# Optimization experiments

Measured on AMD Instinct MI355X. Metric: run time of the kernel, lower is better.

The kernel has to match this reference:

```python
import jax, jax.numpy as jnp
import numpy as np

B, M, N, K = 2, 25000, 100000, 16
HID, DIM, NGROUPS = 64, 64, 8
GN_EPS = 1e-5


def conv1x1(x, w, b):
    # x: [B,C,M,K], w: [O,C], b: [O]
    return jnp.einsum('bcmk,oc->bomk', x, w) + b[None, :, None, None]


def group_norm(x, gamma, beta, ngroups):
    b, c, m, k = x.shape
    xg = x.reshape(b, ngroups, c // ngroups, m, k)
    mu = xg.mean(axis=(2, 3, 4), keepdims=True)
    var = xg.var(axis=(2, 3, 4), keepdims=True)
    xn = ((xg - mu) / jnp.sqrt(var + GN_EPS)).reshape(b, c, m, k)
    return xn * gamma[None, :, None, None] + beta[None, :, None, None]


def mlp(x, w1, b1, g, be, w2, b2):
    h = jax.nn.relu(group_norm(conv1x1(x, w1, b1), g, be, NGROUPS))
    return conv1x1(h, w2, b2)


def setup_inputs() -> dict:
    key = jax.random.key(0)
    ks = jax.random.split(key, 16)
    inp = {
        'q_xyzs': jax.random.normal(ks[0], (B, 3, M), jnp.float32),
        'k_xyzs': jax.random.normal(ks[1], (B, 3, N), jnp.float32),
        'knn_idx': jax.random.randint(ks[2], (B, M, K), 0, N),
        'mask': jax.random.randint(ks[3], (B, M, K), 0, 2).astype(bool),
        # embed_positions MLP params
        'pe_w1': jax.random.normal(ks[4], (HID, 4), jnp.float32) * 0.05,
        'pe_b1': jnp.zeros((HID,), jnp.float32),
        'pe_g': jnp.ones((HID,), jnp.float32),
        'pe_be': jnp.zeros((HID,), jnp.float32),
        'pe_w2': jax.random.normal(ks[5], (DIM, HID), jnp.float32) * 0.05,
        'pe_b2': jnp.zeros((DIM,), jnp.float32),
        # attention MLP params
        'at_w1': jax.random.normal(ks[6], (HID, DIM), jnp.float32) * 0.05,
        'at_b1': jnp.zeros((HID,), jnp.float32),
        'at_g': jnp.ones((HID,), jnp.float32),
        'at_be': jnp.zeros((HID,), jnp.float32),
        'at_w2': jax.random.normal(ks[7], (DIM, HID), jnp.float32) * 0.05,
        'at_b2': jnp.zeros((DIM,), jnp.float32),
    }
    return inp


def reference(q_xyzs, k_xyzs, knn_idx, mask,
              pe_w1, pe_b1, pe_g, pe_be, pe_w2, pe_b2,
              at_w1, at_b1, at_g, at_be, at_w2, at_b2):
    # gather KNN coordinates: [B,3,M,K]
    knn_xyzs = jax.vmap(lambda pts, idx: pts[:, idx])(k_xyzs, knn_idx)
    offset = knn_xyzs - q_xyzs[..., None]
    dist = jnp.linalg.norm(offset, axis=1, keepdims=True)  # [B,1,M,K]
    direction = offset / jnp.maximum(dist, 1e-12)
    local_pattern = jnp.concatenate([direction, dist], axis=1)  # [B,4,M,K]

    pe = mlp(local_pattern, pe_w1, pe_b1, pe_g, pe_be, pe_w2, pe_b2)  # [B,DIM,M,K]
    attn = mlp(pe, at_w1, at_b1, at_g, at_be, at_w2, at_b2)
    mask_value = -jnp.finfo(attn.dtype).max
    attn = jnp.where(mask[:, None], attn, mask_value)
    attn = jax.nn.softmax(attn, axis=-1)
    return (pe * attn).sum(axis=-1)  # [B,DIM,M]
```

## Files before the change

### kernel.cpp

```cpp
#include <hip/hip_runtime.h>

#define Bn 2
#define Mn 25000
#define Nn 100000
#define MK 400000
#define GN_EPS 1e-5f
#define NEG_BIG (-3.402823466e+38f)
#define LOG2E 1.44269504088896340736f

#define G1 512
#define G2 512

#define BEFF_OFF 0
#define B1P_OFF  64
#define AB1P_OFF 192
#define AB2L_OFF 320
#define WF16_OFF 384
#define AW1P_OFF 6528
#define W1F_OFF  10624
#define MSK_OFF  11136
#define SP_OFF   36160
#define YP_OFF   52544
#define YS_OFF   183616
#define KXT_OFF  184128
#define QT_OFF   984128
#define XF_OFF   1184128

typedef _Float16 hf8 __attribute__((ext_vector_type(8)));
typedef _Float16 hf4 __attribute__((ext_vector_type(4)));
typedef _Float16 hf2 __attribute__((ext_vector_type(2)));
typedef float f32x16 __attribute__((ext_vector_type(16)));

__device__ __forceinline__ f32x16 mfma16(hf8 a, hf8 b, f32x16 c) {
    return __builtin_amdgcn_mfma_f32_32x32x16_f16(a, b, c, 0, 0, 0);
}
__device__ __forceinline__ f32x16 splat16(float v) {
    f32x16 x;
#pragma unroll
    for (int r = 0; r < 16; ++r) x[r] = v;
    return x;
}
__device__ __forceinline__ hf8 zero8() {
    hf8 z;
#pragma unroll
    for (int j = 0; j < 8; ++j) z[j] = (_Float16)0.f;
    return z;
}
__device__ __forceinline__ hf2 pkcvt(float a, float b) {
    return __builtin_bit_cast(hf2, __builtin_amdgcn_cvt_pkrtz(a, b));
}
__device__ __forceinline__ hf2 pkrelu(hf2 v) {
    hf2 z; z[0] = (_Float16)0.f; z[1] = (_Float16)0.f;
    return __builtin_elementwise_max(v, z);
}
__device__ __forceinline__ float waveSum(float v) {
#pragma unroll
    for (int s = 32; s; s >>= 1) v += __shfl_down(v, s, 64);
    return v;
}
#define ROWFN(r, lane) (((r) & 3) + 8*((r) >> 2) + 4*((lane) >> 5))

__global__ __launch_bounds__(256) void prep0_kernel(
    const float* __restrict__ q, const float* __restrict__ kx,
    float* __restrict__ ws)
{
    float4* kxt = (float4*)(ws + KXT_OFF);
    float4* qt  = (float4*)(ws + QT_OFF);
    for (int e = blockIdx.x*256 + threadIdx.x; e < 2*Nn; e += gridDim.x*256) {
        const int b = e / Nn, n = e % Nn;
        float4 v;
        v.x = kx[(b*3+0)*Nn + n]; v.y = kx[(b*3+1)*Nn + n];
        v.z = kx[(b*3+2)*Nn + n]; v.w = 0.f;
        kxt[e] = v;
    }
    for (int e = blockIdx.x*256 + threadIdx.x; e < 2*Mn; e += gridDim.x*256) {
        const int b = e / Mn, m = e % Mn;
        float4 v;
        v.x = q[(b*3+0)*Mn + m]; v.y = q[(b*3+1)*Mn + m];
        v.z = q[(b*3+2)*Mn + m]; v.w = 0.f;
        qt[e] = v;
    }
}

__global__ __launch_bounds__(256) void gatherx_kernel(
    const int* __restrict__ idx, const int* __restrict__ mask,
    float* __restrict__ ws)
{
    __shared__ float red[4][16];
    const int b = blockIdx.y;
    const float4* kxt = (const float4*)(ws + KXT_OFF) + (size_t)b*Nn;
    const float4* qt  = (const float4*)(ws + QT_OFF)  + (size_t)b*Mn;
    _Float16* xf = (_Float16*)(ws + XF_OFF);
    unsigned short* m16 = (unsigned short*)(ws + MSK_OFF) + (size_t)b*25024;
    float v[14];
#pragma unroll
    for (int j = 0; j < 14; ++j) v[j] = 0.f;

    for (int i = blockIdx.x*256 + threadIdx.x; i < MK; i += G1*256) {
        const int mm = i >> 4;
        const int id = idx[(size_t)b*MK + i];
        const float4 kv = kxt[id];
        const float4 qv = qt[mm];
        const float ox = kv.x - qv.x, oy = kv.y - qv.y, oz = kv.z - qv.z;
        const float d  = sqrtf(ox*ox + oy*oy + oz*oz);
        const float inv = 1.0f / fmaxf(d, 1e-12f);
        const float x0 = ox*inv, x1 = oy*inv, x2 = oz*inv, x3 = d;

        const hf2 lo = pkcvt(x0, x1);
        const hf2 hi = pkcvt(x2, x3);
        hf4 pk;
        pk[0] = lo[0]; pk[1] = lo[1]; pk[2] = hi[0]; pk[3] = hi[1];
        *(hf4*)&xf[((size_t)b*MK + i)*4] = pk;

        const unsigned long long mb = __ballot(mask[(size_t)b*MK + i] != 0);
        if ((threadIdx.x & 63) == 0)
            *(unsigned long long*)&m16[i >> 4] = mb;

        v[0] += x0; v[1] += x1; v[2] += x2; v[3] += x3;
        v[4] += x0*x0; v[5] += x0*x1; v[6] += x0*x2; v[7] += x0*x3;
        v[8] += x1*x1; v[9] += x1*x2; v[10] += x1*x3;
        v[11] += x2*x2; v[12] += x2*x3; v[13] += x3*x3;
    }
    const int lane = threadIdx.x & 63, wv = threadIdx.x >> 6;
#pragma unroll
    for (int j = 0; j < 14; ++j) v[j] = waveSum(v[j]);
    if (lane == 0) {
#pragma unroll
        for (int j = 0; j < 14; ++j) red[wv][j] = v[j];
    }
    __syncthreads();
    if (threadIdx.x < 14)
        ws[SP_OFF + ((size_t)b*G1 + blockIdx.x)*16 + threadIdx.x] =
            red[0][threadIdx.x] + red[1][threadIdx.x] + red[2][threadIdx.x] + red[3][threadIdx.x];
}

__global__ void prep1_kernel(
    const float* __restrict__ ws_r,
    const float* __restrict__ w1, const float* __restrict__ b1,
    const float* __restrict__ g1, const float* __restrict__ be1,
    const float* __restrict__ w2, const float* __restrict__ pe_b2,
    const float* __restrict__ aw1, const float* __restrict__ ab1,
    const float* __restrict__ aw2, const float* __restrict__ ab2,
    float* __restrict__ ws)
{
    const int t = threadIdx.x;
    _Float16* WF = (_Float16*)(ws + WF16_OFF);

    if (blockIdx.x > 0) {
        const int e = (blockIdx.x - 1)*256 + t;
        const int o = e >> 6, c = e & 63;
        WF[e]        = (_Float16)w2[e];
        WF[4096 + e] = (_Float16)(aw2[e] * LOG2E);
        float acc = 0.f;
        for (int d = 0; d < 64; ++d) acc = fmaf(aw1[o*64 + d], w2[d*64 + c], acc);
        WF[8192 + e] = (_Float16)acc;
        return;
    }

    __shared__ double S[2][14];
    __shared__ float Eh[2][64], Eq[2][64];

    if (t < 28) {
        const int b = t / 14, j = t % 14;
        const float* p = ws_r + SP_OFF + (size_t)b*G1*16 + j;
        double acc = 0.0;
        for (int g = 0; g < G1; g += 4)
            acc += (double)p[(g+0)*16] + (double)p[(g+1)*16]
                 + (double)p[(g+2)*16] + (double)p[(g+3)*16];
        S[b][j] = acc;
    }
    __syncthreads();

    if (t < 128) {
        const int b = t >> 6, o = t & 63;
        const double inv = 1.0 / (double)MK;
        double mu[4];
#pragma unroll
        for (int c = 0; c < 4; ++c) mu[c] = S[b][c] * inv;
        double m2[4][4];
        {
            const int map[4][4] = {{0,1,2,3},{1,4,5,6},{2,5,7,8},{3,6,8,9}};
#pragma unroll
            for (int c = 0; c < 4; ++c)
#pragma unroll
                for (int c2 = 0; c2 < 4; ++c2)
                    m2[c][c2] = S[b][4 + map[c][c2]] * inv;
        }
        double w[4];
#pragma unroll
        for (int c = 0; c < 4; ++c) w[c] = (double)w1[o*4 + c];
        double s = 0.0, qd = 0.0;
#pragma unroll
        for (int c = 0; c < 4; ++c) {
            s += w[c] * mu[c];
#pragma unroll
            for (int c2 = 0; c2 < 4; ++c2) qd += w[c]*w[c2]*m2[c][c2];
        }
        const double bb = (double)b1[o];
        Eh[b][o] = (float)(s + bb);
        Eq[b][o] = (float)(qd + 2.0*bb*s + bb*bb);
    }
    __syncthreads();
    if (t < 128) {
        const int b = t >> 6, o = t & 63, g = o & ~7;
        float mg = 0.f, qg = 0.f;
#pragma unroll
        for (int j = 0; j < 8; ++j) { mg += Eh[b][g + j]; qg += Eq[b][g + j]; }
        mg *= 0.125f; qg *= 0.125f;
        const float var = fmaxf(qg - mg*mg, 0.f);
        const float a = g1[o] / sqrtf(var + GN_EPS);
        const float c1v = be1[o] - mg*a;
        _Float16* W1F = (_Float16*)(ws + W1F_OFF);
        hf8 wrow;
#pragma unroll
        for (int c = 0; c < 4; ++c) wrow[c] = (_Float16)(a * w1[o*4 + c]);
#pragma unroll
        for (int c = 4; c < 8; ++c) wrow[c] = (_Float16)0.f;
        *(hf8*)&W1F[(b*64 + o)*8] = wrow;
        ws[B1P_OFF + b*64 + o] = fmaf(a, b1[o], c1v);
    }
    if (t < 64) {
        float acc = ab1[t];
        for (int d = 0; d < 64; ++d) acc = fmaf(aw1[t*64 + d], pe_b2[d], acc);
        ws[BEFF_OFF + t] = acc;
    } else if (t < 128) {
        ws[AB2L_OFF + (t - 64)] = ab2[t - 64] * LOG2E;
    }
}

__global__ __launch_bounds__(256, 4) void pass2_kernel(
    const float* __restrict__ cws, float* __restrict__ ws)
{
    __shared__ __align__(16) _Float16 Xs[4][32][72];
    const int b = blockIdx.y;
    const int tid = threadIdx.x, lane = tid & 63, wv = tid >> 6;
    const int colA = lane & 31;
    const int klo = (lane >> 5) * 8;
    const _Float16* xf  = (const _Float16*)(cws + XF_OFF);
    const _Float16* WFe = (const _Float16*)(cws + WF16_OFF) + 8192;
    const _Float16* W1F = (const _Float16*)(cws + W1F_OFF);

    hf8 BW[2][4];
#pragma unroll
    for (int jc = 0; jc < 2; ++jc)
#pragma unroll
        for (int ks = 0; ks < 4; ++ks)
            BW[jc][ks] = *(const hf8*)&WFe[(2*colA + jc)*64 + 16*ks + klo];
    hf8 BX[2];
    if (klo == 0) {
        BX[0] = *(const hf8*)&W1F[(b*64 + 2*colA)*8];
        BX[1] = *(const hf8*)&W1F[(b*64 + 2*colA + 1)*8];
    } else { BX[0] = zero8(); BX[1] = zero8(); }
    const float bias0 = cws[B1P_OFF + b*64 + 2*colA];
    const float bias1 = cws[B1P_OFF + b*64 + 2*colA + 1];

    float sh[2] = {0.f, 0.f}, sq[2] = {0.f, 0.f};

    for (int base = blockIdx.x * 128; base < MK; base += G2 * 128) {
        const int pt0 = base + 32*wv;
        hf8 ax = zero8();
        if (klo == 0) {
            hf4 xv = *(const hf4*)&xf[((size_t)b*MK + pt0 + colA)*4];
#pragma unroll
            for (int j = 0; j < 4; ++j) ax[j] = xv[j];
        }
        f32x16 r0 = splat16(bias0), r1t = splat16(bias1);
        r0  = mfma16(ax, BX[0], r0);
        r1t = mfma16(ax, BX[1], r1t);
#pragma unroll
        for (int r = 0; r < 16; ++r) {
            const int row = ROWFN(r, lane);
            *(hf2*)&Xs[wv][row][2*colA] = pkrelu(pkcvt(r0[r], r1t[r]));
        }
        hf8 A[4];
#pragma unroll
        for (int ks = 0; ks < 4; ++ks)
            A[ks] = *(const hf8*)&Xs[wv][colA][16*ks + klo];
#pragma unroll
        for (int jc = 0; jc < 2; ++jc) {
            f32x16 C = splat16(0.f);
#pragma unroll
            for (int ks = 0; ks < 4; ++ks) C = mfma16(A[ks], BW[jc][ks], C);
#pragma unroll
            for (int r = 0; r < 16; ++r) {
                const float vy = C[r];
                sh[jc] += vy;
                sq[jc] = fmaf(vy, vy, sq[jc]);
            }
        }
    }

#pragma unroll
    for (int jc = 0; jc < 2; ++jc) {
        sh[jc] += __shfl_xor(sh[jc], 32, 64);
        sq[jc] += __shfl_xor(sq[jc], 32, 64);
    }
    __syncthreads();
    float* red = (float*)Xs;
    if (lane < 32) {
#pragma unroll
        for (int jc = 0; jc < 2; ++jc) {
            red[wv*128 +      2*colA + jc] = sh[jc];
            red[wv*128 + 64 + 2*colA + jc] = sq[jc];
        }
    }
    __syncthreads();
    if (tid < 128) {
        const float v = red[tid] + red[128 + tid] + red[256 + tid] + red[384 + tid];
        ws[YP_OFF + ((size_t)b*G2 + blockIdx.x)*128 + tid] = v;
    }
}

__global__ __launch_bounds__(64) void prep2a_kernel(
    const float* __restrict__ ws_r, float* __restrict__ ws)
{
    const int o2 = blockIdx.x;
    const int b = o2 >> 7, i = o2 & 127;
    const float* p = ws_r + YP_OFF + (size_t)b*G2*128 + i;
    double acc = 0.0;
    for (int g = threadIdx.x; g < G2; g += 64) acc += (double)p[(size_t)g*128];
#pragma unroll
    for (int s = 32; s; s >>= 1) acc += __shfl_down(acc, s, 64);
    if (threadIdx.x == 0) ((double*)(ws + YS_OFF))[o2] = acc;
}

__global__ void prep2b_kernel(const float* __restrict__ ws_r,
                              const float* __restrict__ g2, const float* __restrict__ be2,
                              const float* __restrict__ aw1, const float* __restrict__ ab1,
                              float* __restrict__ ws)
{
    __shared__ float EH[2][64], EQ[2][64];
    __shared__ float A2s[2][64];
    const int t = threadIdx.x;
    const double* YS = (const double*)(ws_r + YS_OFF);
    if (t < 128) {
        const int b = t >> 6, o = t & 63;
        const double invMK = 1.0 / (double)MK;
        const double my = YS[b*128 + o] * invMK;
        const double qy = YS[b*128 + 64 + o] * invMK;
        const double beff = (double)ws_r[BEFF_OFF + o];
        EH[b][o] = (float)(my + beff);
        EQ[b][o] = (float)(qy + 2.0*beff*my + beff*beff);
    }
    __syncthreads();
    if (t < 128) {
        const int b = t >> 6, o = t & 63, g = o & ~7;
        float mg = 0.f, qg = 0.f;
#pragma unroll
        for (int j = 0; j < 8; ++j) { mg += EH[b][g + j]; qg += EQ[b][g + j]; }
        mg *= 0.125f; qg *= 0.125f;
        const float var = fmaxf(qg - mg*mg, 0.f);
        const float a = g2[o] / sqrtf(var + GN_EPS);
        A2s[b][o] = a;
        ws[AB1P_OFF + b*64 + o] = fmaf(a, ab1[o], be2[o] - mg*a);
    }
    __syncthreads();
    _Float16* AW1P = (_Float16*)(ws + AW1P_OFF);
    for (int e = t; e < 8192; e += 256) {
        const int b = e >> 12, oc = e & 4095, o = oc >> 6;
        AW1P[e] = (_Float16)(A2s[b][o] * aw1[oc]);
    }
}

__global__ __launch_bounds__(256, 4) void pass3_kernel(
    const float* __restrict__ b2,
    const float* __restrict__ cws, float* __restrict__ out)
{
    __shared__ __align__(16) _Float16 Xs[4][32][72];
    float* O = (float*)Xs;

    const int b = blockIdx.y;
    const int base = blockIdx.x * 128;
    const int tid = threadIdx.x;
    const int lane = tid & 63, wv = tid >> 6;
    const int colA = lane & 31;
    const int klo = (lane >> 5) * 8;
    const int pt0 = base + 32*wv;

    const _Float16* xf   = (const _Float16*)(cws + XF_OFF);
    const _Float16* WF   = (const _Float16*)(cws + WF16_OFF);
    const _Float16* AW1P = (const _Float16*)(cws + AW1P_OFF) + (size_t)b*4096;
    const _Float16* W1F  = (const _Float16*)(cws + W1F_OFF);
    const unsigned mb32 = *(const unsigned*)((const unsigned short*)(cws + MSK_OFF)
                                             + (size_t)b*25024 + (pt0 >> 4));
    const unsigned mbs = __builtin_amdgcn_readfirstlane(mb32);

    {
        hf8 ax = zero8();
        hf8 BX0, BX1;
        if (klo == 0) {
            hf4 xv = *(const hf4*)&xf[((size_t)b*MK + pt0 + colA)*4];
#pragma unroll
            for (int j = 0; j < 4; ++j) ax[j] = xv[j];
            BX0 = *(const hf8*)&W1F[(b*64 + 2*colA)*8];
            BX1 = *(const hf8*)&W1F[(b*64 + 2*colA + 1)*8];
        } else { BX0 = zero8(); BX1 = zero8(); }
        f32x16 r0  = splat16(cws[B1P_OFF + b*64 + 2*colA]);
        f32x16 r1t = splat16(cws[B1P_OFF + b*64 + 2*colA + 1]);
        r0  = mfma16(ax, BX0, r0);
        r1t = mfma16(ax, BX1, r1t);
#pragma unroll
        for (int r = 0; r < 16; ++r) {
            const int row = ROWFN(r, lane);
            *(hf2*)&Xs[wv][row][2*colA] = pkrelu(pkcvt(r0[r], r1t[r]));
        }
    }
    if (lane < 32) {
        hf8 pad = zero8();
        pad[0] = ((mb32 >> lane) & 1u) ? (_Float16)0.f : (_Float16)(-60000.f);
        *(hf8*)&Xs[wv][lane][64] = pad;
    }

    f32x16 pe0 = splat16(b2[2*colA]);
    f32x16 pe1 = splat16(b2[2*colA + 1]);
#pragma unroll
    for (int ks = 0; ks < 4; ++ks) {
        const int off = 16*ks + klo;
        hf8 a   = *(const hf8*)&Xs[wv][colA][off];
        hf8 b0f = *(const hf8*)&WF[(2*colA)*64 + off];
        hf8 b1f = *(const hf8*)&WF[(2*colA + 1)*64 + off];
        pe0 = mfma16(a, b0f, pe0);
        pe1 = mfma16(a, b1f, pe1);
    }
#pragma unroll
    for (int r = 0; r < 16; ++r) {
        const int row = ROWFN(r, lane);
        *(hf2*)&Xs[wv][row][2*colA] = pkcvt(pe0[r], pe1[r]);
    }

    f32x16 h0 = splat16(cws[AB1P_OFF + b*64 + 2*colA]);
    f32x16 h1 = splat16(cws[AB1P_OFF + b*64 + 2*colA + 1]);
#pragma unroll
    for (int ks = 0; ks < 4; ++ks) {
        const int off = 16*ks + klo;
        hf8 a   = *(const hf8*)&Xs[wv][colA][off];
        hf8 b0f = *(const hf8*)&AW1P[(2*colA)*64 + off];
        hf8 b1f = *(const hf8*)&AW1P[(2*colA + 1)*64 + off];
        h0 = mfma16(a, b0f, h0);
        h1 = mfma16(a, b1f, h1);
    }
#pragma unroll
    for (int r = 0; r < 16; ++r) {
        const int row = ROWFN(r, lane);
        *(hf2*)&Xs[wv][row][2*colA] = pkrelu(pkcvt(h0[r], h1[r]));
    }

    f32x16 l0 = splat16(cws[AB2L_OFF + 2*colA]);
    f32x16 l1 = splat16(cws[AB2L_OFF + 2*colA + 1]);
#pragma unroll
    for (int ks = 0; ks < 4; ++ks) {
        const int off = 16*ks + klo;
        hf8 a   = *(const hf8*)&Xs[wv][colA][off];
        hf8 b0f = *(const hf8*)&WF[4096 + (2*colA)*64 + off];
        hf8 b1f = *(const hf8*)&WF[4096 + (2*colA + 1)*64 + off];
        l0 = mfma16(a, b0f, l0);
        l1 = mfma16(a, b1f, l1);
    }
    {
        hf8 a5 = zero8(), b5 = zero8();
        if (klo == 0) {
            a5 = *(const hf8*)&Xs[wv][colA][64];
            b5[0] = (_Float16)1.f;
        }
        l0 = mfma16(a5, b5, l0);
        l1 = mfma16(a5, b5, l1);
    }

    __syncthreads();

    {
        auto softmax_tile = [&](const f32x16& lg, const f32x16& pe, int j) {
#pragma unroll
            for (int mh = 0; mh < 2; ++mh) {
                float mx = lg[8*mh];
#pragma unroll
                for (int rr = 1; rr < 8; ++rr) mx = fmaxf(mx, lg[8*mh + rr]);
                mx = fmaxf(mx, __shfl_xor(mx, 32, 64));
                float se, sw = 0.f;
                if (((mbs >> (16*mh)) & 0xFFFFu) != 0u) {
                    se = 0.f;
#pragma unroll
                    for (int rr = 0; rr < 8; ++rr) {
                        const float e = exp2f(lg[8*mh + rr] - mx);
                        se += e;
                        sw = fmaf(e, pe[8*mh + rr], sw);
                    }
                } else {
                    se = 8.f;
#pragma unroll
                    for (int rr = 0; rr < 8; ++rr) sw += pe[8*mh + rr];
                }
                se += __shfl_xor(se, 32, 64);
                sw += __shfl_xor(sw, 32, 64);
                if (lane < 32)
                    O[(2*lane + j)*9 + (2*wv + mh)] = sw * __builtin_amdgcn_rcpf(se);
            }
        };
        softmax_tile(l0, pe0, 0);
        softmax_tile(l1, pe1, 1);
    }
    __syncthreads();

    if (tid < 128) {
        const int o = tid >> 1, mq = (tid & 1) * 4;
        float4 v;
        v.x = O[o*9 + mq];     v.y = O[o*9 + mq + 1];
        v.z = O[o*9 + mq + 2]; v.w = O[o*9 + mq + 3];
        *(float4*)&out[((size_t)b*64 + o)*Mn + blockIdx.x*8 + mq] = v;
    }
}

extern "C" void kernel_launch(void* const* d_in, const int* in_sizes, int n_in,
                              void* d_out, int out_size, void* d_ws, size_t ws_size,
                              hipStream_t stream) {
    (void)in_sizes; (void)n_in; (void)out_size; (void)ws_size;
    const float* q    = (const float*)d_in[0];
    const float* kx   = (const float*)d_in[1];
    const int*   idx  = (const int*)  d_in[2];
    const int*   mask = (const int*)  d_in[3];
    const float* w1   = (const float*)d_in[4];
    const float* b1   = (const float*)d_in[5];
    const float* g1   = (const float*)d_in[6];
    const float* be1  = (const float*)d_in[7];
    const float* w2   = (const float*)d_in[8];
    const float* b2   = (const float*)d_in[9];
    const float* aw1  = (const float*)d_in[10];
    const float* ab1  = (const float*)d_in[11];
    const float* g2   = (const float*)d_in[12];
    const float* be2  = (const float*)d_in[13];
    const float* aw2  = (const float*)d_in[14];
    const float* ab2  = (const float*)d_in[15];
    float* out = (float*)d_out;
    float* ws  = (float*)d_ws;

    prep0_kernel<<<256, 256, 0, stream>>>(q, kx, ws);
    gatherx_kernel<<<dim3(G1, Bn), 256, 0, stream>>>(idx, mask, ws);
    prep1_kernel<<<17, 256, 0, stream>>>(ws, w1, b1, g1, be1, w2, b2, aw1, ab1, aw2, ab2, ws);
    pass2_kernel<<<dim3(G2, Bn), 256, 0, stream>>>(ws, ws);
    prep2a_kernel<<<256, 64, 0, stream>>>(ws, ws);
    prep2b_kernel<<<1, 256, 0, stream>>>(ws, g2, be2, aw1, ab1, ws);
    pass3_kernel<<<dim3(MK/128, Bn), 256, 0, stream>>>(b2, ws, out);
}
```

Before: 221.7 us.

## Process two 32-point tiles per wave in pass3 to reuse weight fragments

Each wave in the final fused MLP/softmax kernel now handles two 32-row tiles (256 points per block instead of 128). The weight B-fragments loaded from global memory are reused across both tiles, and the pe values are kept in packed half registers instead of fp32 accumulators. This halves the grid size and the per-point weight loads, at the cost of more registers (launch bounds reduced to 3 blocks per CU), double the shared memory, and a bounds-checked tail block.

```diff
diff --git a/kernel.cpp b/kernel.cpp
--- a/kernel.cpp
+++ b/kernel.cpp
@@ -362,114 +362,153 @@
     }
 }
 
-__global__ __launch_bounds__(256, 4) void pass3_kernel(
+__global__ __launch_bounds__(256, 3) void pass3_kernel(
     const float* __restrict__ b2,
     const float* __restrict__ cws, float* __restrict__ out)
 {
-    __shared__ __align__(16) _Float16 Xs[4][32][72];
+    __shared__ __align__(16) _Float16 Xs[8][32][72];
     float* O = (float*)Xs;
 
     const int b = blockIdx.y;
-    const int base = blockIdx.x * 128;
+    const int base = blockIdx.x * 256;
     const int tid = threadIdx.x;
     const int lane = tid & 63, wv = tid >> 6;
     const int colA = lane & 31;
     const int klo = (lane >> 5) * 8;
-    const int pt0 = base + 32*wv;
 
     const _Float16* xf   = (const _Float16*)(cws + XF_OFF);
     const _Float16* WF   = (const _Float16*)(cws + WF16_OFF);
     const _Float16* AW1P = (const _Float16*)(cws + AW1P_OFF) + (size_t)b*4096;
     const _Float16* W1F  = (const _Float16*)(cws + W1F_OFF);
-    const unsigned mb32 = *(const unsigned*)((const unsigned short*)(cws + MSK_OFF)
-                                             + (size_t)b*25024 + (pt0 >> 4));
-    const unsigned mbs = __builtin_amdgcn_readfirstlane(mb32);
+    const unsigned short* m16 = (const unsigned short*)(cws + MSK_OFF) + (size_t)b*25024;
+
+    int pt0[2];
+    pt0[0] = base + 64*wv;
+    pt0[1] = base + 64*wv + 32;
+    unsigned mb[2];
+#pragma unroll
+    for (int t = 0; t < 2; ++t)
+        mb[t] = (pt0[t] < MK) ? *(const unsigned*)(m16 + (pt0[t] >> 4)) : 0u;
+    const unsigned mbs0 = __builtin_amdgcn_readfirstlane(mb[0]);
+    const unsigned mbs1 = __builtin_amdgcn_readfirstlane(mb[1]);
 
     {
-        hf8 ax = zero8();
         hf8 BX0, BX1;
         if (klo == 0) {
-            hf4 xv = *(const hf4*)&xf[((size_t)b*MK + pt0 + colA)*4];
-#pragma unroll
-            for (int j = 0; j < 4; ++j) ax[j] = xv[j];
             BX0 = *(const hf8*)&W1F[(b*64 + 2*colA)*8];
             BX1 = *(const hf8*)&W1F[(b*64 + 2*colA + 1)*8];
         } else { BX0 = zero8(); BX1 = zero8(); }
-        f32x16 r0  = splat16(cws[B1P_OFF + b*64 + 2*colA]);
-        f32x16 r1t = splat16(cws[B1P_OFF + b*64 + 2*colA + 1]);
-        r0  = mfma16(ax, BX0, r0);
-        r1t = mfma16(ax, BX1, r1t);
+        const float bias0 = cws[B1P_OFF + b*64 + 2*colA];
+        const float bias1 = cws[B1P_OFF + b*64 + 2*colA + 1];
+#pragma unroll
+        for (int t = 0; t < 2; ++t) {
+            hf8 ax = zero8();
+            if (klo == 0 && pt0[t] < MK) {
+                hf4 xv = *(const hf4*)&xf[((size_t)b*MK + pt0[t] + colA)*4];
+#pragma unroll
+                for (int j = 0; j < 4; ++j) ax[j] = xv[j];
+            }
+            f32x16 r0 = splat16(bias0), r1t = splat16(bias1);
+            r0  = mfma16(ax, BX0, r0);
+            r1t = mfma16(ax, BX1, r1t);
+#pragma unroll
+            for (int r = 0; r < 16; ++r) {
+                const int row = ROWFN(r, lane);
+                *(hf2*)&Xs[2*wv + t][row][2*colA] = pkrelu(pkcvt(r0[r], r1t[r]));
+            }
+            if (lane < 32) {
+                hf8 pad = zero8();
+                pad[0] = ((mb[t] >> lane) & 1u) ? (_Float16)0.f : (_Float16)(-60000.f);
+                *(hf8*)&Xs[2*wv + t][lane][64] = pad;
+            }
+        }
+    }
+
+    hf2 pe_pk[2][16];
+    {
+        f32x16 p00 = splat16(b2[2*colA]);
+        f32x16 p01 = splat16(b2[2*colA + 1]);
+        f32x16 p10 = p00, p11 = p01;
+#pragma unroll
+        for (int ks = 0; ks < 4; ++ks) {
+            const int off = 16*ks + klo;
+            hf8 a0  = *(const hf8*)&Xs[2*wv    ][colA][off];
+            hf8 a1  = *(const hf8*)&Xs[2*wv + 1][colA][off];
+            hf8 b0f = *(const hf8*)&WF[(2*colA)*64 + off];
+            hf8 b1f = *(const hf8*)&WF[(2*colA + 1)*64 + off];
+            p00 = mfma16(a0, b0f, p00);
+            p01 = mfma16(a0, b1f, p01);
+            p10 = mfma16(a1, b0f, p10);
+            p11 = mfma16(a1, b1f, p11);
+        }
 #pragma unroll
         for (int r = 0; r < 16; ++r) {
             const int row = ROWFN(r, lane);
-            *(hf2*)&Xs[wv][row][2*colA] = pkrelu(pkcvt(r0[r], r1t[r]));
-        }
-    }
-    if (lane < 32) {
-        hf8 pad = zero8();
-        pad[0] = ((mb32 >> lane) & 1u) ? (_Float16)0.f : (_Float16)(-60000.f);
-        *(hf8*)&Xs[wv][lane][64] = pad;
-    }
-
-    f32x16 pe0 = splat16(b2[2*colA]);
-    f32x16 pe1 = splat16(b2[2*colA + 1]);
+            pe_pk[0][r] = pkcvt(p00[r], p01[r]);
+            pe_pk[1][r] = pkcvt(p10[r], p11[r]);
+            *(hf2*)&Xs[2*wv    ][row][2*colA] = pe_pk[0][r];
+            *(hf2*)&Xs[2*wv + 1][row][2*colA] = pe_pk[1][r];
+        }
+    }
+
+    {
+        f32x16 h00 = splat16(cws[AB1P_OFF + b*64 + 2*colA]);
+        f32x16 h01 = splat16(cws[AB1P_OFF + b*64 + 2*colA + 1]);
+        f32x16 h10 = h00, h11 = h01;
+#pragma unroll
+        for (int ks = 0; ks < 4; ++ks) {
+            const int off = 16*ks + klo;
+            hf8 a0  = *(const hf8*)&Xs[2*wv    ][colA][off];
+            hf8 a1  = *(const hf8*)&Xs[2*wv + 1][colA][off];
+            hf8 b0f = *(const hf8*)&AW1P[(2*colA)*64 + off];
+            hf8 b1f = *(const hf8*)&AW1P[(2*colA + 1)*64 + off];
+            h00 = mfma16(a0, b0f, h00);
+            h01 = mfma16(a0, b1f, h01);
+            h10 = mfma16(a1, b0f, h10);
+            h11 = mfma16(a1, b1f, h11);
+        }
+#pragma unroll
+        for (int r = 0; r < 16; ++r) {
+            const int row = ROWFN(r, lane);
+            *(hf2*)&Xs[2*wv    ][row][2*colA] = pkrelu(pkcvt(h00[r], h01[r]));
+            *(hf2*)&Xs[2*wv + 1][row][2*colA] = pkrelu(pkcvt(h10[r], h11[r]));
+        }
+    }
+
+    f32x16 l00 = splat16(cws[AB2L_OFF + 2*colA]);
+    f32x16 l01 = splat16(cws[AB2L_OFF + 2*colA + 1]);
+    f32x16 l10 = l00, l11 = l01;
 #pragma unroll
     for (int ks = 0; ks < 4; ++ks) {
         const int off = 16*ks + klo;
-        hf8 a   = *(const hf8*)&Xs[wv][colA][off];
-        hf8 b0f = *(const hf8*)&WF[(2*colA)*64 + off];
-        hf8 b1f = *(const hf8*)&WF[(2*colA + 1)*64 + off];
-        pe0 = mfma16(a, b0f, pe0);
-        pe1 = mfma16(a, b1f, pe1);
-    }
-#pragma unroll
-    for (int r = 0; r < 16; ++r) {
-        const int row = ROWFN(r, lane);
-        *(hf2*)&Xs[wv][row][2*colA] = pkcvt(pe0[r], pe1[r]);
-    }
-
-    f32x16 h0 = splat16(cws[AB1P_OFF + b*64 + 2*colA]);
-    f32x16 h1 = splat16(cws[AB1P_OFF + b*64 + 2*colA + 1]);
-#pragma unroll
-    for (int ks = 0; ks < 4; ++ks) {
-        const int off = 16*ks + klo;
-        hf8 a   = *(const hf8*)&Xs[wv][colA][off];
-        hf8 b0f = *(const hf8*)&AW1P[(2*colA)*64 + off];
-        hf8 b1f = *(const hf8*)&AW1P[(2*colA + 1)*64 + off];
-        h0 = mfma16(a, b0f, h0);
-        h1 = mfma16(a, b1f, h1);
-    }
-#pragma unroll
-    for (int r = 0; r < 16; ++r) {
-        const int row = ROWFN(r, lane);
-        *(hf2*)&Xs[wv][row][2*colA] = pkrelu(pkcvt(h0[r], h1[r]));
-    }
-
-    f32x16 l0 = splat16(cws[AB2L_OFF + 2*colA]);
-    f32x16 l1 = splat16(cws[AB2L_OFF + 2*colA + 1]);
-#pragma unroll
-    for (int ks = 0; ks < 4; ++ks) {
-        const int off = 16*ks + klo;
-        hf8 a   = *(const hf8*)&Xs[wv][colA][off];
+        hf8 a0  = *(const hf8*)&Xs[2*wv    ][colA][off];
+        hf8 a1  = *(const hf8*)&Xs[2*wv + 1][colA][off];
         hf8 b0f = *(const hf8*)&WF[4096 + (2*colA)*64 + off];
         hf8 b1f = *(const hf8*)&WF[4096 + (2*colA + 1)*64 + off];
-        l0 = mfma16(a, b0f, l0);
-        l1 = mfma16(a, b1f, l1);
+        l00 = mfma16(a0, b0f, l00);
+        l01 = mfma16(a0, b1f, l01);
+        l10 = mfma16(a1, b0f, l10);
+        l11 = mfma16(a1, b1f, l11);
     }
     {
-        hf8 a5 = zero8(), b5 = zero8();
+        hf8 b5 = zero8();
+        if (klo == 0) b5[0] = (_Float16)1.f;
+        hf8 a50 = zero8(), a51 = zero8();
         if (klo == 0) {
-            a5 = *(const hf8*)&Xs[wv][colA][64];
-            b5[0] = (_Float16)1.f;
-        }
-        l0 = mfma16(a5, b5, l0);
-        l1 = mfma16(a5, b5, l1);
+            a50 = *(const hf8*)&Xs[2*wv    ][colA][64];
+            a51 = *(const hf8*)&Xs[2*wv + 1][colA][64];
+        }
+        l00 = mfma16(a50, b5, l00);
+        l01 = mfma16(a50, b5, l01);
+        l10 = mfma16(a51, b5, l10);
+        l11 = mfma16(a51, b5, l11);
     }
 
     __syncthreads();
 
     {
-        auto softmax_tile = [&](const f32x16& lg, const f32x16& pe, int j) {
+        auto softmax_tile = [&](const f32x16& lg, const hf2* pp, unsigned mbst,
+                                int t, int j) {
 #pragma unroll
             for (int mh = 0; mh < 2; ++mh) {
                 float mx = lg[8*mh];
@@ -477,36 +516,41 @@
                 for (int rr = 1; rr < 8; ++rr) mx = fmaxf(mx, lg[8*mh + rr]);
                 mx = fmaxf(mx, __shfl_xor(mx, 32, 64));
                 float se, sw = 0.f;
-                if (((mbs >> (16*mh)) & 0xFFFFu) != 0u) {
+                if (((mbst >> (16*mh)) & 0xFFFFu) != 0u) {
                     se = 0.f;
 #pragma unroll
                     for (int rr = 0; rr < 8; ++rr) {
                         const float e = exp2f(lg[8*mh + rr] - mx);
                         se += e;
-                        sw = fmaf(e, pe[8*mh + rr], sw);
+                        sw = fmaf(e, (float)pp[8*mh + rr][j], sw);
                     }
                 } else {
                     se = 8.f;
 #pragma unroll
-                    for (int rr = 0; rr < 8; ++rr) sw += pe[8*mh + rr];
+                    for (int rr = 0; rr < 8; ++rr) sw += (float)pp[8*mh + rr][j];
                 }
                 se += __shfl_xor(se, 32, 64);
                 sw += __shfl_xor(sw, 32, 64);
                 if (lane < 32)
-                    O[(2*lane + j)*9 + (2*wv + mh)] = sw * __builtin_amdgcn_rcpf(se);
+                    O[(2*lane + j)*17 + (4*wv + 2*t + mh)] = sw * __builtin_amdgcn_rcpf(se);
             }
         };
-        softmax_tile(l0, pe0, 0);
-        softmax_tile(l1, pe1, 1);
-    }
-    __syncthreads();
-
-    if (tid < 128) {
-        const int o = tid >> 1, mq = (tid & 1) * 4;
-        float4 v;
-        v.x = O[o*9 + mq];     v.y = O[o*9 + mq + 1];
-        v.z = O[o*9 + mq + 2]; v.w = O[o*9 + mq + 3];
-        *(float4*)&out[((size_t)b*64 + o)*Mn + blockIdx.x*8 + mq] = v;
+        softmax_tile(l00, pe_pk[0], mbs0, 0, 0);
+        softmax_tile(l01, pe_pk[0], mbs0, 0, 1);
+        softmax_tile(l10, pe_pk[1], mbs1, 1, 0);
+        softmax_tile(l11, pe_pk[1], mbs1, 1, 1);
+    }
+    __syncthreads();
+
+    {
+        const int o = tid >> 2, mq = (tid & 3) * 4;
+        const int m0 = blockIdx.x * 16;
+        if (m0 + mq < Mn) {
+            float4 v;
+            v.x = O[o*17 + mq];     v.y = O[o*17 + mq + 1];
+            v.z = O[o*17 + mq + 2]; v.w = O[o*17 + mq + 3];
+            *(float4*)&out[((size_t)b*64 + o)*Mn + m0 + mq] = v;
+        }
     }
 }
 
@@ -539,5 +583,5 @@
     pass2_kernel<<<dim3(G2, Bn), 256, 0, stream>>>(ws, ws);
     prep2a_kernel<<<256, 64, 0, stream>>>(ws, ws);
     prep2b_kernel<<<1, 256, 0, stream>>>(ws, g2, be2, aw1, ab1, ws);
-    pass3_kernel<<<dim3(MK/128, Bn), 256, 0, stream>>>(b2, ws, out);
-}
+    pass3_kernel<<<dim3((MK + 255)/256, Bn), 256, 0, stream>>>(b2, ws, out);
+}
```

Result: faster. 194.3 us (median of 2 runs) (-12.4%).
